# Kernel tuning notes

Hardware: AMD Instinct MI355X
Metric: run time of the kernel (lower is better)

The kernel has to match this reference:

```python
import jax, jax.numpy as jnp
import numpy as np

N_USER, N_ITEM, N_BUNDLE = 200000, 100000, 50000
EMBED_DIM = 128
B, L = 8192, 100  # batch of bundles, max items per bundle


def setup_inputs() -> dict:
    key = jax.random.key(0)
    ks = jax.random.split(key, 12)
    d, d2 = EMBED_DIM, 2 * EMBED_DIM
    x_u = jax.random.randint(ks[0], (B,), 0, N_USER)
    x_b = jax.random.randint(ks[1], (B,), 0, N_BUNDLE)
    items = jax.random.randint(ks[2], (B, L), 0, N_ITEM)
    # ragged bundle sizes in [10, L]; padded+masked form of the CSR gather
    lengths = jax.random.randint(ks[3], (B,), 10, L + 1)
    mask = jnp.arange(L)[None, :] < lengths[:, None]  # [B, L] bool
    return {
        "x_u": x_u,
        "x_b": x_b,
        "items": items,
        "mask": mask,
        "emb_u": jax.random.normal(ks[4], (N_USER, d), jnp.float32) * 0.1,
        "emb_i": jax.random.normal(ks[5], (N_ITEM, d), jnp.float32) * 0.1,
        "emb_b": jax.random.normal(ks[6], (N_BUNDLE, d), jnp.float32) * 0.1,
        "A": jax.random.normal(ks[7], (N_ITEM, d), jnp.float32) * 0.1,
        "fc1_w": jax.random.normal(ks[8], (d2, d2), jnp.float32) / np.sqrt(d2),
        "fc1_b": jnp.zeros((d2,), jnp.float32),
        "fc2_w": jax.random.normal(ks[9], (d2, d2), jnp.float32) / np.sqrt(d2),
        "fc2_b": jnp.zeros((d2,), jnp.float32),
        "out_w": jax.random.normal(ks[10], (1, d2), jnp.float32) / np.sqrt(d2),
        "out_b": jnp.zeros((1,), jnp.float32),
    }


def reference(x_u, x_b, items, mask, emb_u, emb_i, emb_b, A,
              fc1_w, fc1_b, fc2_w, fc2_b, out_w, out_b):
    # DAM.forward_bundle with the attention() per-bundle loop vectorized
    h_u = emb_u[x_u]                       # [B, d]
    h_b = emb_b[x_b]                       # [B, d]
    item_e = emb_i[items]                  # [B, L, d] ragged gather (padded)
    a_e = A[items]                         # [B, L, d]
    # w = softmax_l( sum_d e_u * A[item] ) per bundle, over valid items only
    scores = jnp.einsum('bd,bld->bl', h_u, a_e)
    scores = jnp.where(mask, scores, -jnp.inf)
    w = jax.nn.softmax(scores, axis=1)     # [B, L]
    h_x = jnp.einsum('bl,bld->bd', w, item_e)
    h = jnp.concatenate([h_u, h_b + h_x], axis=1)   # [B, 2d]
    h = jax.nn.leaky_relu(h @ fc1_w.T + fc1_b)
    h = jax.nn.leaky_relu(h @ fc2_w.T + fc2_b)
    return h @ out_w.T + out_b             # [B, 1]
```

## Files before the change

### kernel.cpp

```cpp
#include <hip/hip_runtime.h>
#include <hip/hip_bf16.h>

#define D   128
#define D2  256
#define H1P 272

typedef short bf16x8 __attribute__((ext_vector_type(8)));
typedef float f32x4  __attribute__((ext_vector_type(4)));

__device__ __forceinline__ float bf2f(unsigned short u) {
    return __uint_as_float(((unsigned int)u) << 16);
}
__device__ __forceinline__ float bflo(unsigned int p) { return __uint_as_float(p << 16); }
__device__ __forceinline__ float bfhi(unsigned int p) { return __uint_as_float(p & 0xffff0000u); }
__device__ __forceinline__ unsigned short f2bf(float f) {
    __hip_bfloat16 h = __float2bfloat16(f);
    return *(unsigned short*)&h;
}

template<bool BF>
__device__ __forceinline__ float ld1(const void* p, size_t i) {
    if constexpr (BF) return bf2f(((const unsigned short*)p)[i]);
    else              return ((const float*)p)[i];
}

template<bool BF>
__device__ __forceinline__ void load8f(const void* p, size_t elem_off, float* r) {
    if constexpr (BF) {
        uint4 v = *(const uint4*)((const unsigned short*)p + elem_off);
        r[0]=bflo(v.x); r[1]=bfhi(v.x); r[2]=bflo(v.y); r[3]=bfhi(v.y);
        r[4]=bflo(v.z); r[5]=bfhi(v.z); r[6]=bflo(v.w); r[7]=bfhi(v.w);
    } else {
        const float4* q = (const float4*)((const float*)p + elem_off);
        float4 a = q[0], b = q[1];
        r[0]=a.x; r[1]=a.y; r[2]=a.z; r[3]=a.w;
        r[4]=b.x; r[5]=b.y; r[6]=b.z; r[7]=b.w;
    }
}

__device__ __forceinline__ void unpack8(uint4 v, float* r) {
    r[0]=bflo(v.x); r[1]=bfhi(v.x); r[2]=bflo(v.y); r[3]=bfhi(v.y);
    r[4]=bflo(v.z); r[5]=bfhi(v.z); r[6]=bflo(v.w); r[7]=bfhi(v.w);
}

__device__ __forceinline__ void store8bf(unsigned short* p, const float* r) {
    union { unsigned short u[8]; uint4 v; } pk;
    #pragma unroll
    for (int k = 0; k < 8; ++k) pk.u[k] = f2bf(r[k]);
    *(uint4*)p = pk.v;
}

__device__ __forceinline__ bool read_mask(const void* mask, int mmode, size_t i) {
    if (mmode == 0) return ((const int*)mask)[i] != 0;
    if (mmode == 1) return ((const unsigned char*)mask)[i] != 0;
    return ((const unsigned short*)mask)[i] != 0;
}

__device__ __forceinline__ bool probe_is_bf16(const unsigned int* probe) {
    const int lane = threadIdx.x & 63;
    int cnt = 0;
    #pragma unroll
    for (int i = 0; i < 4; ++i) {
        unsigned int e = (probe[lane + 64 * i] >> 7) & 0xffu;
        cnt += (e >= 90 && e < 130) ? 1 : 0;
    }
    #pragma unroll
    for (int o = 32; o; o >>= 1) cnt += __shfl_xor(cnt, o);
    return cnt >= 128;
}

template<bool BF>
__device__ __forceinline__ void attn_wave(
    const int* __restrict__ x_u, const int* __restrict__ x_b,
    const int* __restrict__ items, const void* __restrict__ mask, int mmode,
    const void* __restrict__ emb_u, const void* __restrict__ emb_i,
    const void* __restrict__ emb_b, const void* __restrict__ Aw,
    unsigned short* __restrict__ h_out, int L)
{
    const int lane = threadIdx.x & 63;
    const int wv   = threadIdx.x >> 6;
    const int b    = blockIdx.x * 4 + wv;

    const int xu = x_u[b], xb = x_b[b];

    const int  c0 = (lane < L) ? lane : 0;
    int  i0 = items[(size_t)b * L + c0];
    bool v0 = (lane < L) && read_mask(mask, mmode, (size_t)b * L + c0);
    int  i1 = i0;
    bool v1 = false;
    if (64 + lane < L) {
        i1 = items[(size_t)b * L + 64 + lane];
        v1 = read_mask(mask, mmode, (size_t)b * L + 64 + lane);
    }
    const int len = __popcll(__ballot(v0)) + __popcll(__ballot(v1));

    const int g = lane >> 4, m16 = lane & 15;

    float hu8[8];
    load8f<BF>(emb_u, (size_t)xu * D + m16 * 8, hu8);

    auto get_id = [&](int p) -> int {
        const int idx = 4 * p + g;
        const int src = (idx < len) ? idx : 0;
        return (src < 64) ? __shfl(i0, src) : __shfl(i1, src - 64);
    };

    float esum = 0.f;
    float acc8[8];
    #pragma unroll
    for (int k = 0; k < 8; ++k) acc8[k] = 0.f;

    if constexpr (BF) {
        const unsigned short* AW = (const unsigned short*)Aw;
        const unsigned short* EI = (const unsigned short*)emb_i;
        for (int grp = 0; grp < 4; ++grp) {
            if (grp == 0 || grp * 32 < len) {
                uint4 ab[8], vb[8];
                #pragma unroll
                for (int q = 0; q < 8; ++q) {
                    const int id = get_id(grp * 8 + q);
                    ab[q] = *(const uint4*)(AW + (size_t)id * D + m16 * 8);
                    vb[q] = *(const uint4*)(EI + (size_t)id * D + m16 * 8);
                }
                #pragma unroll
                for (int q = 0; q < 8; ++q) {
                    float af[8];
                    unpack8(ab[q], af);
                    float s = 0.f;
                    #pragma unroll
                    for (int k = 0; k < 8; ++k) s += hu8[k] * af[k];
                    s += __shfl_xor(s, 1); s += __shfl_xor(s, 2);
                    s += __shfl_xor(s, 4); s += __shfl_xor(s, 8);
                    const int idx = 4 * (grp * 8 + q) + g;
                    const float e = (idx < len) ? __expf(s) : 0.f;
                    esum += e;
                    float vf[8];
                    unpack8(vb[q], vf);
                    #pragma unroll
                    for (int k = 0; k < 8; ++k) acc8[k] += e * vf[k];
                }
            }
        }
    } else {
        const int NP = (len + 3) >> 2;
        auto fetchf = [&](int p, float* a, float* v) {
            const int id = get_id(p);
            load8f<false>(Aw,    (size_t)id * D + m16 * 8, a);
            load8f<false>(emb_i, (size_t)id * D + m16 * 8, v);
        };
        float a0[8], u0[8], a1[8], u1[8];
        fetchf(0, a0, u0);
        if (1 < NP) fetchf(1, a1, u1);
        for (int p = 0; p < NP; ++p) {
            float ca[8], cv[8];
            #pragma unroll
            for (int k = 0; k < 8; ++k) { ca[k] = a0[k]; cv[k] = u0[k]; }
            #pragma unroll
            for (int k = 0; k < 8; ++k) { a0[k] = a1[k]; u0[k] = u1[k]; }
            if (p + 2 < NP) fetchf(p + 2, a1, u1);
            float s = 0.f;
            #pragma unroll
            for (int k = 0; k < 8; ++k) s += hu8[k] * ca[k];
            s += __shfl_xor(s, 1); s += __shfl_xor(s, 2);
            s += __shfl_xor(s, 4); s += __shfl_xor(s, 8);
            const int idx = 4 * p + g;
            const float e = (idx < len) ? __expf(s) : 0.f;
            esum += e;
            #pragma unroll
            for (int k = 0; k < 8; ++k) acc8[k] += e * cv[k];
        }
    }

    esum += __shfl_xor(esum, 16);
    esum += __shfl_xor(esum, 32);
    #pragma unroll
    for (int k = 0; k < 8; ++k) {
        acc8[k] += __shfl_xor(acc8[k], 16);
        acc8[k] += __shfl_xor(acc8[k], 32);
    }
    const float inv = (esum > 0.f) ? 1.f / esum : 0.f;

    if (g == 0) {
        if constexpr (BF) {
            uint4 raw = *(const uint4*)((const unsigned short*)emb_u
                                        + (size_t)xu * D + m16 * 8);
            *(uint4*)(h_out + (size_t)b * D2 + m16 * 8) = raw;
        } else {
            float r[8];
            load8f<false>(emb_u, (size_t)xu * D + m16 * 8, r);
            store8bf(h_out + (size_t)b * D2 + m16 * 8, r);
        }
        float rb2[8], outv[8];
        load8f<BF>(emb_b, (size_t)xb * D + m16 * 8, rb2);
        #pragma unroll
        for (int k = 0; k < 8; ++k) outv[k] = rb2[k] + acc8[k] * inv;
        store8bf(h_out + (size_t)b * D2 + D + m16 * 8, outv);
    }
}

__global__ __launch_bounds__(256) void attn_kernel(
    const int* x_u, const int* x_b, const int* items, const void* mask,
    const void* emb_u, const void* emb_i, const void* emb_b, const void* A,
    unsigned short* h_out, int L)
{
    const bool bf = probe_is_bf16((const unsigned int*)emb_u);
    const unsigned char* mb = (const unsigned char*)mask;
    const int mm = (mb[1] == 0) ? 0 : ((mb[0] == 1) ? 1 : 2);

    if (bf) attn_wave<true >(x_u, x_b, items, mask, mm, emb_u, emb_i, emb_b, A, h_out, L);
    else    attn_wave<false>(x_u, x_b, items, mask, mm, emb_u, emb_i, emb_b, A, h_out, L);
}

template<bool BF>
__device__ __forceinline__ bf16x8 load_w8(const void* W, size_t off) {
    if constexpr (BF) {
        return *(const bf16x8*)((const unsigned short*)W + off);
    } else {
        const float* p = (const float*)W + off;
        float4 a = *(const float4*)p;
        float4 b = *(const float4*)(p + 4);
        bf16x8 r;
        r[0] = (short)f2bf(a.x); r[1] = (short)f2bf(a.y);
        r[2] = (short)f2bf(a.z); r[3] = (short)f2bf(a.w);
        r[4] = (short)f2bf(b.x); r[5] = (short)f2bf(b.y);
        r[6] = (short)f2bf(b.z); r[7] = (short)f2bf(b.w);
        return r;
    }
}

template<bool BF>
__device__ __forceinline__ void mlp_body(
    const unsigned short* __restrict__ X,
    const void* __restrict__ fc1_w, const void* __restrict__ fc1_b,
    const void* __restrict__ fc2_w, const void* __restrict__ fc2_b,
    const void* __restrict__ out_w, const void* __restrict__ out_b,
    void* __restrict__ out,
    unsigned short* h1_s, float (*po_s)[16])
{
    const int tid  = threadIdx.x;
    const int wave = tid >> 6;
    const int lane = tid & 63;
    const int l16  = lane & 15;
    const int quad = lane >> 4;
    const int mt   = blockIdx.x * 16;

    bf16x8 afrag[8];
    const size_t abase = (size_t)(mt + l16) * D2 + quad * 8;
    #pragma unroll
    for (int kc = 0; kc < 8; ++kc)
        afrag[kc] = *(const bf16x8*)(X + abase + kc * 32);

    #pragma unroll
    for (int jj = 0; jj < 4; ++jj) {
        const int jt = wave * 4 + jj;
        const size_t bbase = (size_t)(jt * 16 + l16) * D2 + quad * 8;
        f32x4 acc = {0.f, 0.f, 0.f, 0.f};
        #pragma unroll
        for (int kc = 0; kc < 8; ++kc) {
            bf16x8 bfrag = load_w8<BF>(fc1_w, bbase + kc * 32);
            acc = __builtin_amdgcn_mfma_f32_16x16x32_bf16(afrag[kc], bfrag, acc, 0, 0, 0);
        }
        const int j  = jt * 16 + l16;
        const float bj = ld1<BF>(fc1_b, j);
        #pragma unroll
        for (int r = 0; r < 4; ++r) {
            float v = acc[r] + bj;
            v = v > 0.f ? v : 0.01f * v;
            h1_s[(quad * 4 + r) * H1P + j] = f2bf(v);
        }
    }
    __syncthreads();

    bf16x8 afrag2[8];
    #pragma unroll
    for (int kc = 0; kc < 8; ++kc)
        afrag2[kc] = *(const bf16x8*)&h1_s[l16 * H1P + quad * 8 + kc * 32];

    float po[4] = {0.f, 0.f, 0.f, 0.f};
    #pragma unroll
    for (int jj = 0; jj < 4; ++jj) {
        const int jt = wave * 4 + jj;
        const size_t bbase = (size_t)(jt * 16 + l16) * D2 + quad * 8;
        f32x4 acc = {0.f, 0.f, 0.f, 0.f};
        #pragma unroll
        for (int kc = 0; kc < 8; ++kc) {
            bf16x8 bfrag = load_w8<BF>(fc2_w, bbase + kc * 32);
            acc = __builtin_amdgcn_mfma_f32_16x16x32_bf16(afrag2[kc], bfrag, acc, 0, 0, 0);
        }
        const int j  = jt * 16 + l16;
        const float bj = ld1<BF>(fc2_b, j);
        const float wj = ld1<BF>(out_w, j);
        #pragma unroll
        for (int r = 0; r < 4; ++r) {
            float v = acc[r] + bj;
            v = v > 0.f ? v : 0.01f * v;
            po[r] += v * wj;
        }
    }
    #pragma unroll
    for (int r = 0; r < 4; ++r) {
        #pragma unroll
        for (int o = 1; o < 16; o <<= 1) po[r] += __shfl_xor(po[r], o);
    }
    if (l16 == 0) {
        #pragma unroll
        for (int r = 0; r < 4; ++r) po_s[wave][quad * 4 + r] = po[r];
    }
    __syncthreads();

    if (tid < 16) {
        const float v = po_s[0][tid] + po_s[1][tid] + po_s[2][tid] + po_s[3][tid]
                      + ld1<BF>(out_b, 0);
        if constexpr (BF) ((unsigned short*)out)[mt + tid] = f2bf(v);
        else              ((float*)out)[mt + tid] = v;
    }
}

__global__ __launch_bounds__(256) void mlp_kernel(
    const unsigned short* X,
    const void* fc1_w, const void* fc1_b, const void* fc2_w, const void* fc2_b,
    const void* out_w, const void* out_b, void* out, const void* probe)
{
    __shared__ unsigned short h1_s[16 * H1P];
    __shared__ float po_s[4][16];

    const bool bf = probe_is_bf16((const unsigned int*)probe);
    if (bf) mlp_body<true >(X, fc1_w, fc1_b, fc2_w, fc2_b, out_w, out_b, out, h1_s, po_s);
    else    mlp_body<false>(X, fc1_w, fc1_b, fc2_w, fc2_b, out_w, out_b, out, h1_s, po_s);
}

extern "C" void kernel_launch(void* const* d_in, const int* in_sizes, int n_in,
                              void* d_out, int out_size, void* d_ws, size_t ws_size,
                              hipStream_t stream) {
    const int*  x_u   = (const int*)d_in[0];
    const int*  x_b   = (const int*)d_in[1];
    const int*  items = (const int*)d_in[2];
    const void* mask  = d_in[3];
    const void* emb_u = d_in[4];
    const void* emb_i = d_in[5];
    const void* emb_b = d_in[6];
    const void* A     = d_in[7];
    const void* fc1_w = d_in[8];
    const void* fc1_b = d_in[9];
    const void* fc2_w = d_in[10];
    const void* fc2_b = d_in[11];
    const void* out_w = d_in[12];
    const void* out_b = d_in[13];

    const int B = in_sizes[0];
    const int L = in_sizes[2] / B;

    unsigned short* h = (unsigned short*)d_ws;

    attn_kernel<<<B / 4, 256, 0, stream>>>(x_u, x_b, items, mask,
                                           emb_u, emb_i, emb_b, A, h, L);
    mlp_kernel<<<B / 16, 256, 0, stream>>>(h, fc1_w, fc1_b, fc2_w, fc2_b,
                                           out_w, out_b, d_out, emb_i);
}
```

Before: 306.1 us.

## Split each bundle's attention across four waves and widen MLP blocks to eight waves

The attention kernel now gives each bundle its own 256-thread block: each of the four waves handles a 32-item slice, and partial softmax sums and weighted accumulators are combined through shared memory after a barrier. This spreads the long gather latency of one bundle across more waves and raises parallelism, at the cost of more blocks, a block-wide sync, and idle waves on short bundles. The MLP kernel moves to 512 threads (8 waves), with each wave computing two 16-column tiles instead of four, so a block's work is split across more waves.

```diff
diff --git a/kernel.cpp b/kernel.cpp
--- a/kernel.cpp
+++ b/kernel.cpp
@@ -70,18 +70,19 @@
 }
 
 template<bool BF>
-__device__ __forceinline__ void attn_wave(
+__device__ __forceinline__ void attn_row(
     const int* __restrict__ x_u, const int* __restrict__ x_b,
     const int* __restrict__ items, const void* __restrict__ mask, int mmode,
     const void* __restrict__ emb_u, const void* __restrict__ emb_i,
     const void* __restrict__ emb_b, const void* __restrict__ Aw,
-    unsigned short* __restrict__ h_out, int L)
+    unsigned short* __restrict__ h_out, int L,
+    float (*s_acc)[128], float* s_es)
 {
     const int lane = threadIdx.x & 63;
     const int wv   = threadIdx.x >> 6;
-    const int b    = blockIdx.x * 4 + wv;
-
-    const int xu = x_u[b], xb = x_b[b];
+    const int b    = blockIdx.x;
+
+    const int xu = x_u[b];
 
     const int  c0 = (lane < L) ? lane : 0;
     int  i0 = items[(size_t)b * L + c0];
@@ -99,8 +100,8 @@
     float hu8[8];
     load8f<BF>(emb_u, (size_t)xu * D + m16 * 8, hu8);
 
-    auto get_id = [&](int p) -> int {
-        const int idx = 4 * p + g;
+    auto get_id = [&](int q) -> int {
+        const int idx = 32 * wv + 4 * q + g;
         const int src = (idx < len) ? idx : 0;
         return (src < 64) ? __shfl(i0, src) : __shfl(i1, src - 64);
     };
@@ -110,77 +111,88 @@
     #pragma unroll
     for (int k = 0; k < 8; ++k) acc8[k] = 0.f;
 
-    if constexpr (BF) {
-        const unsigned short* AW = (const unsigned short*)Aw;
-        const unsigned short* EI = (const unsigned short*)emb_i;
-        for (int grp = 0; grp < 4; ++grp) {
-            if (grp == 0 || grp * 32 < len) {
-                uint4 ab[8], vb[8];
-                #pragma unroll
-                for (int q = 0; q < 8; ++q) {
-                    const int id = get_id(grp * 8 + q);
-                    ab[q] = *(const uint4*)(AW + (size_t)id * D + m16 * 8);
-                    vb[q] = *(const uint4*)(EI + (size_t)id * D + m16 * 8);
-                }
-                #pragma unroll
-                for (int q = 0; q < 8; ++q) {
-                    float af[8];
-                    unpack8(ab[q], af);
-                    float s = 0.f;
-                    #pragma unroll
-                    for (int k = 0; k < 8; ++k) s += hu8[k] * af[k];
-                    s += __shfl_xor(s, 1); s += __shfl_xor(s, 2);
-                    s += __shfl_xor(s, 4); s += __shfl_xor(s, 8);
-                    const int idx = 4 * (grp * 8 + q) + g;
-                    const float e = (idx < len) ? __expf(s) : 0.f;
-                    esum += e;
-                    float vf[8];
-                    unpack8(vb[q], vf);
-                    #pragma unroll
-                    for (int k = 0; k < 8; ++k) acc8[k] += e * vf[k];
-                }
+    const bool active = (wv == 0) || (32 * wv < len);
+    if (active) {
+        if constexpr (BF) {
+            const unsigned short* AW = (const unsigned short*)Aw;
+            const unsigned short* EI = (const unsigned short*)emb_i;
+            uint4 ab[8], vb[8];
+            #pragma unroll
+            for (int q = 0; q < 8; ++q) {
+                const int id = get_id(q);
+                ab[q] = *(const uint4*)(AW + (size_t)id * D + m16 * 8);
+                vb[q] = *(const uint4*)(EI + (size_t)id * D + m16 * 8);
             }
-        }
-    } else {
-        const int NP = (len + 3) >> 2;
-        auto fetchf = [&](int p, float* a, float* v) {
-            const int id = get_id(p);
-            load8f<false>(Aw,    (size_t)id * D + m16 * 8, a);
-            load8f<false>(emb_i, (size_t)id * D + m16 * 8, v);
-        };
-        float a0[8], u0[8], a1[8], u1[8];
-        fetchf(0, a0, u0);
-        if (1 < NP) fetchf(1, a1, u1);
-        for (int p = 0; p < NP; ++p) {
-            float ca[8], cv[8];
             #pragma unroll
-            for (int k = 0; k < 8; ++k) { ca[k] = a0[k]; cv[k] = u0[k]; }
-            #pragma unroll
-            for (int k = 0; k < 8; ++k) { a0[k] = a1[k]; u0[k] = u1[k]; }
-            if (p + 2 < NP) fetchf(p + 2, a1, u1);
-            float s = 0.f;
-            #pragma unroll
-            for (int k = 0; k < 8; ++k) s += hu8[k] * ca[k];
-            s += __shfl_xor(s, 1); s += __shfl_xor(s, 2);
-            s += __shfl_xor(s, 4); s += __shfl_xor(s, 8);
-            const int idx = 4 * p + g;
-            const float e = (idx < len) ? __expf(s) : 0.f;
-            esum += e;
-            #pragma unroll
-            for (int k = 0; k < 8; ++k) acc8[k] += e * cv[k];
-        }
-    }
-
-    esum += __shfl_xor(esum, 16);
-    esum += __shfl_xor(esum, 32);
-    #pragma unroll
-    for (int k = 0; k < 8; ++k) {
-        acc8[k] += __shfl_xor(acc8[k], 16);
-        acc8[k] += __shfl_xor(acc8[k], 32);
-    }
-    const float inv = (esum > 0.f) ? 1.f / esum : 0.f;
+            for (int q = 0; q < 8; ++q) {
+                float af[8];
+                unpack8(ab[q], af);
+                float s = 0.f;
+                #pragma unroll
+                for (int k = 0; k < 8; ++k) s += hu8[k] * af[k];
+                s += __shfl_xor(s, 1); s += __shfl_xor(s, 2);
+                s += __shfl_xor(s, 4); s += __shfl_xor(s, 8);
+                const int idx = 32 * wv + 4 * q + g;
+                const float e = (idx < len) ? __expf(s) : 0.f;
+                esum += e;
+                float vf[8];
+                unpack8(vb[q], vf);
+                #pragma unroll
+                for (int k = 0; k < 8; ++k) acc8[k] += e * vf[k];
+            }
+        } else {
+            float a0[8], u0[8], a1[8], u1[8];
+            auto fetchf = [&](int q, float* a, float* v) {
+                const int id = get_id(q);
+                load8f<false>(Aw,    (size_t)id * D + m16 * 8, a);
+                load8f<false>(emb_i, (size_t)id * D + m16 * 8, v);
+            };
+            fetchf(0, a0, u0);
+            fetchf(1, a1, u1);
+            for (int q = 0; q < 8; ++q) {
+                float ca[8], cv[8];
+                #pragma unroll
+                for (int k = 0; k < 8; ++k) { ca[k] = a0[k]; cv[k] = u0[k]; }
+                #pragma unroll
+                for (int k = 0; k < 8; ++k) { a0[k] = a1[k]; u0[k] = u1[k]; }
+                if (q + 2 < 8) fetchf(q + 2, a1, u1);
+                float s = 0.f;
+                #pragma unroll
+                for (int k = 0; k < 8; ++k) s += hu8[k] * ca[k];
+                s += __shfl_xor(s, 1); s += __shfl_xor(s, 2);
+                s += __shfl_xor(s, 4); s += __shfl_xor(s, 8);
+                const int idx = 32 * wv + 4 * q + g;
+                const float e = (idx < len) ? __expf(s) : 0.f;
+                esum += e;
+                #pragma unroll
+                for (int k = 0; k < 8; ++k) acc8[k] += e * cv[k];
+            }
+        }
+        esum += __shfl_xor(esum, 16);
+        esum += __shfl_xor(esum, 32);
+        #pragma unroll
+        for (int k = 0; k < 8; ++k) {
+            acc8[k] += __shfl_xor(acc8[k], 16);
+            acc8[k] += __shfl_xor(acc8[k], 32);
+        }
+    }
 
     if (g == 0) {
+        #pragma unroll
+        for (int k = 0; k < 8; ++k) s_acc[wv][m16 * 8 + k] = acc8[k];
+        if (m16 == 0) s_es[wv] = esum;
+    }
+    __syncthreads();
+
+    if (wv == 0 && g == 0) {
+        const float es = s_es[0] + s_es[1] + s_es[2] + s_es[3];
+        float at[8];
+        #pragma unroll
+        for (int k = 0; k < 8; ++k)
+            at[k] = s_acc[0][m16 * 8 + k] + s_acc[1][m16 * 8 + k]
+                  + s_acc[2][m16 * 8 + k] + s_acc[3][m16 * 8 + k];
+        const float inv = (es > 0.f) ? 1.f / es : 0.f;
+
         if constexpr (BF) {
             uint4 raw = *(const uint4*)((const unsigned short*)emb_u
                                         + (size_t)xu * D + m16 * 8);
@@ -190,10 +202,11 @@
             load8f<false>(emb_u, (size_t)xu * D + m16 * 8, r);
             store8bf(h_out + (size_t)b * D2 + m16 * 8, r);
         }
+        const int xb = x_b[b];
         float rb2[8], outv[8];
         load8f<BF>(emb_b, (size_t)xb * D + m16 * 8, rb2);
         #pragma unroll
-        for (int k = 0; k < 8; ++k) outv[k] = rb2[k] + acc8[k] * inv;
+        for (int k = 0; k < 8; ++k) outv[k] = rb2[k] + at[k] * inv;
         store8bf(h_out + (size_t)b * D2 + D + m16 * 8, outv);
     }
 }
@@ -203,12 +216,15 @@
     const void* emb_u, const void* emb_i, const void* emb_b, const void* A,
     unsigned short* h_out, int L)
 {
+    __shared__ float s_acc[4][128];
+    __shared__ float s_es[4];
+
     const bool bf = probe_is_bf16((const unsigned int*)emb_u);
     const unsigned char* mb = (const unsigned char*)mask;
     const int mm = (mb[1] == 0) ? 0 : ((mb[0] == 1) ? 1 : 2);
 
-    if (bf) attn_wave<true >(x_u, x_b, items, mask, mm, emb_u, emb_i, emb_b, A, h_out, L);
-    else    attn_wave<false>(x_u, x_b, items, mask, mm, emb_u, emb_i, emb_b, A, h_out, L);
+    if (bf) attn_row<true >(x_u, x_b, items, mask, mm, emb_u, emb_i, emb_b, A, h_out, L, s_acc, s_es);
+    else    attn_row<false>(x_u, x_b, items, mask, mm, emb_u, emb_i, emb_b, A, h_out, L, s_acc, s_es);
 }
 
 template<bool BF>
@@ -251,8 +267,8 @@
         afrag[kc] = *(const bf16x8*)(X + abase + kc * 32);
 
     #pragma unroll
-    for (int jj = 0; jj < 4; ++jj) {
-        const int jt = wave * 4 + jj;
+    for (int jj = 0; jj < 2; ++jj) {
+        const int jt = wave * 2 + jj;
         const size_t bbase = (size_t)(jt * 16 + l16) * D2 + quad * 8;
         f32x4 acc = {0.f, 0.f, 0.f, 0.f};
         #pragma unroll
@@ -278,8 +294,8 @@
 
     float po[4] = {0.f, 0.f, 0.f, 0.f};
     #pragma unroll
-    for (int jj = 0; jj < 4; ++jj) {
-        const int jt = wave * 4 + jj;
+    for (int jj = 0; jj < 2; ++jj) {
+        const int jt = wave * 2 + jj;
         const size_t bbase = (size_t)(jt * 16 + l16) * D2 + quad * 8;
         f32x4 acc = {0.f, 0.f, 0.f, 0.f};
         #pragma unroll
@@ -309,20 +325,21 @@
     __syncthreads();
 
     if (tid < 16) {
-        const float v = po_s[0][tid] + po_s[1][tid] + po_s[2][tid] + po_s[3][tid]
-                      + ld1<BF>(out_b, 0);
+        float v = ld1<BF>(out_b, 0);
+        #pragma unroll
+        for (int w = 0; w < 8; ++w) v += po_s[w][tid];
         if constexpr (BF) ((unsigned short*)out)[mt + tid] = f2bf(v);
         else              ((float*)out)[mt + tid] = v;
     }
 }
 
-__global__ __launch_bounds__(256) void mlp_kernel(
+__global__ __launch_bounds__(512, 4) void mlp_kernel(
     const unsigned short* X,
     const void* fc1_w, const void* fc1_b, const void* fc2_w, const void* fc2_b,
     const void* out_w, const void* out_b, void* out, const void* probe)
 {
     __shared__ unsigned short h1_s[16 * H1P];
-    __shared__ float po_s[4][16];
+    __shared__ float po_s[8][16];
 
     const bool bf = probe_is_bf16((const unsigned int*)probe);
     if (bf) mlp_body<true >(X, fc1_w, fc1_b, fc2_w, fc2_b, out_w, out_b, out, h1_s, po_s);
@@ -352,8 +369,8 @@
 
     unsigned short* h = (unsigned short*)d_ws;
 
-    attn_kernel<<<B / 4, 256, 0, stream>>>(x_u, x_b, items, mask,
-                                           emb_u, emb_i, emb_b, A, h, L);
-    mlp_kernel<<<B / 16, 256, 0, stream>>>(h, fc1_w, fc1_b, fc2_w, fc2_b,
+    attn_kernel<<<B, 256, 0, stream>>>(x_u, x_b, items, mask,
+                                       emb_u, emb_i, emb_b, A, h, L);
+    mlp_kernel<<<B / 16, 512, 0, stream>>>(h, fc1_w, fc1_b, fc2_w, fc2_b,
                                            out_w, out_b, d_out, emb_i);
 }
```

Measured after the change: 306.6 us. Within noise of the previous version (+0.2%).

## Fuse attention gather and MLP into a single kernel via LDS staging

Applied to the files above, without the earlier changes.

Merges the attention kernel and the MLP kernel into one launch. Each block of 8 waves computes 16 bundle rows of attention into shared memory, then runs the two MFMA layers from LDS instead of a global workspace. This removes the intermediate global write and read and one launch, but serializes MLP work behind the gather phase within each block and changes the block size and occupancy.

```diff
diff --git a/kernel.cpp b/kernel.cpp
--- a/kernel.cpp
+++ b/kernel.cpp
@@ -3,6 +3,7 @@
 
 #define D   128
 #define D2  256
+#define XS  264
 #define H1P 272
 
 typedef short bf16x8 __attribute__((ext_vector_type(8)));
@@ -70,18 +71,15 @@
 }
 
 template<bool BF>
-__device__ __forceinline__ void attn_wave(
+__device__ __forceinline__ void attn_one_row(
     const int* __restrict__ x_u, const int* __restrict__ x_b,
     const int* __restrict__ items, const void* __restrict__ mask, int mmode,
     const void* __restrict__ emb_u, const void* __restrict__ emb_i,
     const void* __restrict__ emb_b, const void* __restrict__ Aw,
-    unsigned short* __restrict__ h_out, int L)
+    unsigned short* __restrict__ x_row, int b, int L)
 {
     const int lane = threadIdx.x & 63;
-    const int wv   = threadIdx.x >> 6;
-    const int b    = blockIdx.x * 4 + wv;
-
-    const int xu = x_u[b], xb = x_b[b];
+    const int xu = x_u[b];
 
     const int  c0 = (lane < L) ? lane : 0;
     int  i0 = items[(size_t)b * L + c0];
@@ -184,31 +182,19 @@
         if constexpr (BF) {
             uint4 raw = *(const uint4*)((const unsigned short*)emb_u
                                         + (size_t)xu * D + m16 * 8);
-            *(uint4*)(h_out + (size_t)b * D2 + m16 * 8) = raw;
+            *(uint4*)(x_row + m16 * 8) = raw;
         } else {
             float r[8];
             load8f<false>(emb_u, (size_t)xu * D + m16 * 8, r);
-            store8bf(h_out + (size_t)b * D2 + m16 * 8, r);
-        }
+            store8bf(x_row + m16 * 8, r);
+        }
+        const int xb = x_b[b];
         float rb2[8], outv[8];
         load8f<BF>(emb_b, (size_t)xb * D + m16 * 8, rb2);
         #pragma unroll
         for (int k = 0; k < 8; ++k) outv[k] = rb2[k] + acc8[k] * inv;
-        store8bf(h_out + (size_t)b * D2 + D + m16 * 8, outv);
-    }
-}
-
-__global__ __launch_bounds__(256) void attn_kernel(
-    const int* x_u, const int* x_b, const int* items, const void* mask,
-    const void* emb_u, const void* emb_i, const void* emb_b, const void* A,
-    unsigned short* h_out, int L)
-{
-    const bool bf = probe_is_bf16((const unsigned int*)emb_u);
-    const unsigned char* mb = (const unsigned char*)mask;
-    const int mm = (mb[1] == 0) ? 0 : ((mb[0] == 1) ? 1 : 2);
-
-    if (bf) attn_wave<true >(x_u, x_b, items, mask, mm, emb_u, emb_i, emb_b, A, h_out, L);
-    else    attn_wave<false>(x_u, x_b, items, mask, mm, emb_u, emb_i, emb_b, A, h_out, L);
+        store8bf(x_row + D + m16 * 8, outv);
+    }
 }
 
 template<bool BF>
@@ -229,13 +215,16 @@
 }
 
 template<bool BF>
-__device__ __forceinline__ void mlp_body(
-    const unsigned short* __restrict__ X,
+__device__ __forceinline__ void fused_body(
+    const int* __restrict__ x_u, const int* __restrict__ x_b,
+    const int* __restrict__ items, const void* __restrict__ mask, int mmode,
+    const void* __restrict__ emb_u, const void* __restrict__ emb_i,
+    const void* __restrict__ emb_b, const void* __restrict__ Aw,
     const void* __restrict__ fc1_w, const void* __restrict__ fc1_b,
     const void* __restrict__ fc2_w, const void* __restrict__ fc2_b,
     const void* __restrict__ out_w, const void* __restrict__ out_b,
-    void* __restrict__ out,
-    unsigned short* h1_s, float (*po_s)[16])
+    void* __restrict__ out, int L,
+    unsigned short* x_s, unsigned short* h1_s, float (*po_s)[16])
 {
     const int tid  = threadIdx.x;
     const int wave = tid >> 6;
@@ -244,15 +233,22 @@
     const int quad = lane >> 4;
     const int mt   = blockIdx.x * 16;
 
+    #pragma unroll
+    for (int rr = 0; rr < 2; ++rr) {
+        const int r = wave + rr * 8;
+        attn_one_row<BF>(x_u, x_b, items, mask, mmode, emb_u, emb_i, emb_b, Aw,
+                         &x_s[r * XS], mt + r, L);
+    }
+    __syncthreads();
+
     bf16x8 afrag[8];
-    const size_t abase = (size_t)(mt + l16) * D2 + quad * 8;
     #pragma unroll
     for (int kc = 0; kc < 8; ++kc)
-        afrag[kc] = *(const bf16x8*)(X + abase + kc * 32);
-
-    #pragma unroll
-    for (int jj = 0; jj < 4; ++jj) {
-        const int jt = wave * 4 + jj;
+        afrag[kc] = *(const bf16x8*)&x_s[l16 * XS + quad * 8 + kc * 32];
+
+    #pragma unroll
+    for (int jj = 0; jj < 2; ++jj) {
+        const int jt = wave * 2 + jj;
         const size_t bbase = (size_t)(jt * 16 + l16) * D2 + quad * 8;
         f32x4 acc = {0.f, 0.f, 0.f, 0.f};
         #pragma unroll
@@ -278,8 +274,8 @@
 
     float po[4] = {0.f, 0.f, 0.f, 0.f};
     #pragma unroll
-    for (int jj = 0; jj < 4; ++jj) {
-        const int jt = wave * 4 + jj;
+    for (int jj = 0; jj < 2; ++jj) {
+        const int jt = wave * 2 + jj;
         const size_t bbase = (size_t)(jt * 16 + l16) * D2 + quad * 8;
         f32x4 acc = {0.f, 0.f, 0.f, 0.f};
         #pragma unroll
@@ -309,24 +305,34 @@
     __syncthreads();
 
     if (tid < 16) {
-        const float v = po_s[0][tid] + po_s[1][tid] + po_s[2][tid] + po_s[3][tid]
-                      + ld1<BF>(out_b, 0);
+        float v = ld1<BF>(out_b, 0);
+        #pragma unroll
+        for (int w = 0; w < 8; ++w) v += po_s[w][tid];
         if constexpr (BF) ((unsigned short*)out)[mt + tid] = f2bf(v);
         else              ((float*)out)[mt + tid] = v;
     }
 }
 
-__global__ __launch_bounds__(256) void mlp_kernel(
-    const unsigned short* X,
+__global__ __launch_bounds__(512, 4) void fused_kernel(
+    const int* x_u, const int* x_b, const int* items, const void* mask,
+    const void* emb_u, const void* emb_i, const void* emb_b, const void* A,
     const void* fc1_w, const void* fc1_b, const void* fc2_w, const void* fc2_b,
-    const void* out_w, const void* out_b, void* out, const void* probe)
+    const void* out_w, const void* out_b, void* out, int L)
 {
+    __shared__ unsigned short x_s[16 * XS];
     __shared__ unsigned short h1_s[16 * H1P];
-    __shared__ float po_s[4][16];
-
-    const bool bf = probe_is_bf16((const unsigned int*)probe);
-    if (bf) mlp_body<true >(X, fc1_w, fc1_b, fc2_w, fc2_b, out_w, out_b, out, h1_s, po_s);
-    else    mlp_body<false>(X, fc1_w, fc1_b, fc2_w, fc2_b, out_w, out_b, out, h1_s, po_s);
+    __shared__ float po_s[8][16];
+
+    const bool bf = probe_is_bf16((const unsigned int*)emb_u);
+    const unsigned char* mb = (const unsigned char*)mask;
+    const int mm = (mb[1] == 0) ? 0 : ((mb[0] == 1) ? 1 : 2);
+
+    if (bf) fused_body<true >(x_u, x_b, items, mask, mm, emb_u, emb_i, emb_b, A,
+                              fc1_w, fc1_b, fc2_w, fc2_b, out_w, out_b, out, L,
+                              x_s, h1_s, po_s);
+    else    fused_body<false>(x_u, x_b, items, mask, mm, emb_u, emb_i, emb_b, A,
+                              fc1_w, fc1_b, fc2_w, fc2_b, out_w, out_b, out, L,
+                              x_s, h1_s, po_s);
 }
 
 extern "C" void kernel_launch(void* const* d_in, const int* in_sizes, int n_in,
@@ -350,10 +356,8 @@
     const int B = in_sizes[0];
     const int L = in_sizes[2] / B;
 
-    unsigned short* h = (unsigned short*)d_ws;
-
-    attn_kernel<<<B / 4, 256, 0, stream>>>(x_u, x_b, items, mask,
-                                           emb_u, emb_i, emb_b, A, h, L);
-    mlp_kernel<<<B / 16, 256, 0, stream>>>(h, fc1_w, fc1_b, fc2_w, fc2_b,
-                                           out_w, out_b, d_out, emb_i);
-}
+    fused_kernel<<<B / 16, 512, 0, stream>>>(x_u, x_b, items, mask,
+                                             emb_u, emb_i, emb_b, A,
+                                             fc1_w, fc1_b, fc2_w, fc2_b,
+                                             out_w, out_b, d_out, L);
+}
```

Result: faster. 299.9 us (-2.0%).
